# Kernel optimization log

Hardware: AMD Instinct MI355X
Metric: run time of the kernel (lower is better)

Reference implementation:

```python
import jax, jax.numpy as jnp
import numpy as np

EMBED_DIM = 768
NUM_HEADS = 8
HEAD_DIM = EMBED_DIM // NUM_HEADS
WINDOW_HALF = (17 - 1) // 2          # window_size=17 -> 8
GAP = 3 + 1                          # dilation_gap=3 -> stride 4
OVERLAP = WINDOW_HALF * GAP          # 32
N_LINES = 8192


def setup_inputs() -> dict:
    key = jax.random.key(0)
    k1, k2, k3, k4, k5 = jax.random.split(key, 5)
    D = EMBED_DIM
    return {
        "main": jax.random.normal(k1, (N_LINES, D), dtype=jnp.float32),
        "begin": jax.random.normal(k2, (OVERLAP, D), dtype=jnp.float32),
        "end": jax.random.normal(k3, (OVERLAP, D), dtype=jnp.float32),
        "in_proj_w": jax.random.normal(k4, (3 * D, D), dtype=jnp.float32) * 0.02,
        "in_proj_b": jnp.zeros((3 * D,), dtype=jnp.float32),
        "out_proj_w": jax.random.normal(k5, (D, D), dtype=jnp.float32) * 0.02,
        "out_proj_b": jnp.zeros((D,), dtype=jnp.float32),
    }


def reference(main, begin, end, in_proj_w, in_proj_b, out_proj_w, out_proj_b):
    N, D = main.shape
    H, hd = NUM_HEADS, HEAD_DIM
    # combined buffer [begin | main | end]; the per-token shifted concatenations
    # in the torch loop are equivalent to a strided gather into this buffer.
    combined = jnp.concatenate([begin, main, end], axis=0)  # [N + 2*OVERLAP, D]
    offsets = jnp.concatenate([
        jnp.arange(-OVERLAP, 0, GAP),
        jnp.arange(GAP, OVERLAP + GAP, GAP),
    ])  # [2*WINDOW_HALF] = [16]
    idx = jnp.arange(N)[:, None] + OVERLAP + offsets[None, :]  # [N, W]
    keys = combined[idx]  # [N, W, D] dilated window keys (= values)

    wq, wk, wv = in_proj_w[:D], in_proj_w[D:2 * D], in_proj_w[2 * D:]
    bq, bk, bv = in_proj_b[:D], in_proj_b[D:2 * D], in_proj_b[2 * D:]

    q = (main @ wq.T + bq).reshape(N, H, hd) * (hd ** -0.5)   # [N,H,hd]
    k = (keys @ wk.T + bk).reshape(N, -1, H, hd)              # [N,W,H,hd]
    v = (keys @ wv.T + bv).reshape(N, -1, H, hd)              # [N,W,H,hd]

    scores = jnp.einsum('nhd,nwhd->nhw', q, k)                # [N,H,W]
    attn = jax.nn.softmax(scores, axis=-1)
    ctx = jnp.einsum('nhw,nwhd->nhd', attn, v).reshape(N, D)
    attn_out = ctx @ out_proj_w.T + out_proj_b                # [N,D]
    return jnp.concatenate([main, attn_out], axis=-1)         # [N,2D]
```

## Files before the change

kernel.cpp:

```cpp
#include <hip/hip_runtime.h>
#include <math.h>

#define D 768
#define NQKV 2304
#define NH 8
#define HD 96
#define NW 16
#define OVL 32
#define NLINES 8192
#define NCOMB 8256
#define MPAD 8320
#define CH 64
#define SCALE_Q 0.1020620726159657f
#define COMB_BLOCKS 6240

typedef int i32x8 __attribute__((ext_vector_type(8)));
typedef float f32x4 __attribute__((ext_vector_type(4)));
typedef float f32x2 __attribute__((ext_vector_type(2)));

__device__ __forceinline__ unsigned int pk_fp8x4(float a, float b, float c, float d) {
    int u = __builtin_amdgcn_cvt_pk_fp8_f32(a, b, 0, false);
    u = __builtin_amdgcn_cvt_pk_fp8_f32(c, d, u, true);
    return (unsigned int)u;
}
__device__ __forceinline__ unsigned char f2fp8(float v) {
    return (unsigned char)(__builtin_amdgcn_cvt_pk_fp8_f32(v, v, 0, false) & 0xFF);
}
template <bool HI>
__device__ __forceinline__ f32x2 upk(unsigned int u) {
    return __builtin_amdgcn_cvt_pk_f32_fp8((int)u, HI);
}
__device__ __forceinline__ float dot4f8(unsigned int a, unsigned int b) {
    const f32x2 al = upk<false>(a), ah = upk<true>(a);
    const f32x2 bl = upk<false>(b), bh = upk<true>(b);
    return al.x * bl.x + al.y * bl.y + ah.x * bh.x + ah.y * bh.y;
}

__device__ __forceinline__ void stage16(const void* g, void* l) {
    __builtin_amdgcn_global_load_lds(
        (const __attribute__((address_space(1))) unsigned int*)g,
        (__attribute__((address_space(3))) unsigned int*)l, 16, 0, 0);
}

__device__ __forceinline__ void stage_sw(const unsigned char* gbase, unsigned char* lds, int ch) {
    const int row = ch >> 3;
    const int half = ch & 1;
    const int o = (((ch >> 1) & 3) - row) & 3;
    stage16(gbase + (size_t)row * D + o * 32 + half * 16, lds + ch * 16);
}

__device__ __forceinline__ int xcd_swz(int lin, int nwg) {
    const int q = nwg >> 3, r = nwg & 7;
    const int x = lin & 7, i = lin >> 3;
    return (x < r ? x * (q + 1) : r * (q + 1) + (x - r) * q) + i;
}

__global__ __launch_bounds__(256) void convert_all(const float* __restrict__ main_,
                                                   const float* __restrict__ begin_,
                                                   const float* __restrict__ end_,
                                                   const float* __restrict__ in_w,
                                                   const float* __restrict__ in_b,
                                                   const float* __restrict__ out_w,
                                                   unsigned int* __restrict__ comb_dst,
                                                   unsigned int* __restrict__ w_dst,
                                                   float* __restrict__ bias_s,
                                                   float* __restrict__ out) {
    const int bid = blockIdx.x;
    if (bid < COMB_BLOCKS) {
        const int i = bid * 256 + threadIdx.x;
        const int row = i / 192, c4 = i % 192;
        float4 v = make_float4(0.f, 0.f, 0.f, 0.f);
        if (row < NCOMB) {
            const float* src = (row < OVL) ? begin_ + (size_t)row * D
                             : (row < OVL + NLINES) ? main_ + (size_t)(row - OVL) * D
                                                    : end_ + (size_t)(row - OVL - NLINES) * D;
            v = *(const float4*)(src + c4 * 4);
            if (row >= OVL && row < OVL + NLINES)
                *(float4*)(out + (size_t)(row - OVL) * (2 * D) + c4 * 4) = v;
        }
        comb_dst[(size_t)row * 192 + c4] = pk_fp8x4(v.x, v.y, v.z, v.w);
    } else {
        const int j = (bid - COMB_BLOCKS) * 256 + threadIdx.x;
        const int f0 = j * 4;
        const bool is_out = f0 >= 3 * D * D;
        const float4 v = is_out ? *(const float4*)(out_w + (f0 - 3 * D * D))
                                : *(const float4*)(in_w + f0);
        const float s = 16.0f * ((f0 < D * D) ? SCALE_Q : 1.0f);
        w_dst[j] = pk_fp8x4(v.x * s, v.y * s, v.z * s, v.w * s);
        if (bid == COMB_BLOCKS) {
            for (int b = threadIdx.x; b < NQKV; b += 256)
                bias_s[b] = in_b[b] * (b < D ? SCALE_Q : 1.0f);
        }
    }
}

__global__ __launch_bounds__(256) void qkv_gemm(const unsigned char* __restrict__ comb,
                                                const unsigned char* __restrict__ w_f8,
                                                const float* __restrict__ bias_s,
                                                unsigned char* __restrict__ Qb,
                                                unsigned char* __restrict__ Kb,
                                                unsigned char* __restrict__ Vb) {
    __shared__ __align__(16) unsigned char As[2][128 * 128];
    __shared__ __align__(16) unsigned char Bs[2][128 * 128];
    const int lin = blockIdx.y * 18 + blockIdx.x;
    const int s = xcd_swz(lin, 18 * 65);
    const int bx = s % 18;
    const int m0 = (s / 18) * 128;
    const int n0 = bx * 128;
    const int tid = threadIdx.x;
    const int lane = tid & 63;
    const int wave = tid >> 6;
    const int wm = (wave & 1) * 64, wn = (wave >> 1) * 64;
    const int q = lane >> 4, l15 = lane & 15;
    const int swq = (q + l15) & 3;

#pragma unroll
    for (int it = 0; it < 4; it++) {
        const int ch = tid + it * 256;
        stage_sw(comb + (size_t)m0 * D, As[0], ch);
        stage_sw(w_f8 + (size_t)n0 * D, Bs[0], ch);
    }

    f32x4 acc[4][4] = {};
    int cur = 0;
    for (int k0 = 0; k0 < D; k0 += 128) {
        if (k0 + 128 < D) {
#pragma unroll
            for (int it = 0; it < 4; it++) {
                const int ch = tid + it * 256;
                stage_sw(comb + (size_t)m0 * D + k0 + 128, As[cur ^ 1], ch);
                stage_sw(w_f8 + (size_t)n0 * D + k0 + 128, Bs[cur ^ 1], ch);
            }
            asm volatile("s_waitcnt vmcnt(8)" ::: "memory");
        } else {
            asm volatile("s_waitcnt vmcnt(0)" ::: "memory");
        }
        __builtin_amdgcn_sched_barrier(0);
        __builtin_amdgcn_s_barrier();
        __builtin_amdgcn_sched_barrier(0);

        i32x8 af[4], bfr[4];
#pragma unroll
        for (int i = 0; i < 4; i++)
            af[i] = *(const i32x8*)(As[cur] + (wm + i * 16 + l15) * 128 + swq * 32);
#pragma unroll
        for (int j = 0; j < 4; j++)
            bfr[j] = *(const i32x8*)(Bs[cur] + (wn + j * 16 + l15) * 128 + swq * 32);
#pragma unroll
        for (int i = 0; i < 4; i++)
#pragma unroll
            for (int j = 0; j < 4; j++)
                acc[i][j] = __builtin_amdgcn_mfma_scale_f32_16x16x128_f8f6f4(
                    af[i], bfr[j], acc[i][j], 0, 0, 0, 127, 0, 123);

        asm volatile("s_waitcnt lgkmcnt(0)" ::: "memory");
        __builtin_amdgcn_sched_barrier(0);
        __builtin_amdgcn_s_barrier();
        __builtin_amdgcn_sched_barrier(0);
        cur ^= 1;
    }

    unsigned char* Cb = (bx < 6) ? Qb : (bx < 12 ? Kb : Vb);
    const int nloc = (bx % 6) * 128;
#pragma unroll
    for (int i = 0; i < 4; i++)
#pragma unroll
        for (int j = 0; j < 4; j++)
#pragma unroll
            for (int r = 0; r < 4; r++) {
                const int row = m0 + wm + i * 16 + q * 4 + r;
                const int col = wn + j * 16 + l15;
                Cb[(size_t)row * D + nloc + col] = f2fp8(acc[i][j][r] + bias_s[bx * 128 + col]);
            }
}

__global__ __launch_bounds__(256) void out_gemm(const unsigned char* __restrict__ ctx,
                                                const unsigned char* __restrict__ w,
                                                const float* __restrict__ bias,
                                                float* __restrict__ out) {
    __shared__ __align__(16) unsigned char As[2][64 * 128];
    __shared__ __align__(16) unsigned char Bs[2][128 * 128];
    const int lin = blockIdx.y * 6 + blockIdx.x;
    const int s = xcd_swz(lin, 6 * 128);
    const int m0 = (s / 6) * 64;
    const int n0 = (s % 6) * 128;
    const int tid = threadIdx.x;
    const int lane = tid & 63;
    const int wave = tid >> 6;
    const int wn = wave * 32;
    const int q = lane >> 4, l15 = lane & 15;
    const int swq = (q + l15) & 3;

#pragma unroll
    for (int it = 0; it < 2; it++)
        stage_sw(ctx + (size_t)m0 * D, As[0], tid + it * 256);
#pragma unroll
    for (int it = 0; it < 4; it++)
        stage_sw(w + (size_t)n0 * D, Bs[0], tid + it * 256);

    f32x4 acc[4][2] = {};
    int cur = 0;
    for (int k0 = 0; k0 < D; k0 += 128) {
        if (k0 + 128 < D) {
#pragma unroll
            for (int it = 0; it < 2; it++)
                stage_sw(ctx + (size_t)m0 * D + k0 + 128, As[cur ^ 1], tid + it * 256);
#pragma unroll
            for (int it = 0; it < 4; it++)
                stage_sw(w + (size_t)n0 * D + k0 + 128, Bs[cur ^ 1], tid + it * 256);
            asm volatile("s_waitcnt vmcnt(6)" ::: "memory");
        } else {
            asm volatile("s_waitcnt vmcnt(0)" ::: "memory");
        }
        __builtin_amdgcn_sched_barrier(0);
        __builtin_amdgcn_s_barrier();
        __builtin_amdgcn_sched_barrier(0);

        i32x8 af[4], bfr[2];
#pragma unroll
        for (int i = 0; i < 4; i++)
            af[i] = *(const i32x8*)(As[cur] + (i * 16 + l15) * 128 + swq * 32);
#pragma unroll
        for (int j = 0; j < 2; j++)
            bfr[j] = *(const i32x8*)(Bs[cur] + (wn + j * 16 + l15) * 128 + swq * 32);
#pragma unroll
        for (int i = 0; i < 4; i++)
#pragma unroll
            for (int j = 0; j < 2; j++)
                acc[i][j] = __builtin_amdgcn_mfma_scale_f32_16x16x128_f8f6f4(
                    af[i], bfr[j], acc[i][j], 0, 0, 0, 127, 0, 123);

        asm volatile("s_waitcnt lgkmcnt(0)" ::: "memory");
        __builtin_amdgcn_sched_barrier(0);
        __builtin_amdgcn_s_barrier();
        __builtin_amdgcn_sched_barrier(0);
        cur ^= 1;
    }

#pragma unroll
    for (int i = 0; i < 4; i++)
#pragma unroll
        for (int j = 0; j < 2; j++)
#pragma unroll
            for (int r = 0; r < 4; r++) {
                const int row = m0 + i * 16 + q * 4 + r;
                const int col = n0 + wn + j * 16 + l15;
                out[(size_t)row * (2 * D) + D + col] = acc[i][j][r] + bias[col];
            }
}

__global__ __launch_bounds__(256) void attn_kernel(const unsigned char* __restrict__ Q,
                                                   const unsigned char* __restrict__ K,
                                                   const unsigned char* __restrict__ V,
                                                   unsigned char* __restrict__ ctx) {
    const int lin = blockIdx.y * 128 + blockIdx.x;
    const int s = xcd_swz(lin, 128 * 8);
    const int n0 = (s % 128) * CH;
    const int h = s / 128;
    const int tid = threadIdx.x;

    __shared__ __align__(16) unsigned char sK[128 * 128];
    __shared__ __align__(16) unsigned char sV[128 * 128];
    __shared__ float sS[CH][17];

    const int l = tid & 63;
    const int wg = tid >> 6;

#pragma unroll
    for (int it = 0; it < 3; it++) {
        const int idx = tid + it * 256;
        const int row = idx / 6, c = idx % 6;
        const int slot = (c + row) & 7;
        *(uint4*)(sK + row * 128 + slot * 16) =
            *(const uint4*)(K + (size_t)(n0 + row) * D + h * HD + c * 16);
        *(uint4*)(sV + row * 128 + slot * 16) =
            *(const uint4*)(V + (size_t)(n0 + row) * D + h * HD + c * 16);
    }
    uint4 qreg[6];
#pragma unroll
    for (int c = 0; c < 6; c++)
        qreg[c] = *(const uint4*)(Q + (size_t)(n0 + l) * D + h * HD + c * 16);
    __syncthreads();

#pragma unroll
    for (int wi = 0; wi < 4; wi++) {
        const int w = wg * 4 + wi;
        const int lrow = l + 4 * w + (w >= 8 ? 4 : 0);
        float sc = 0.f;
#pragma unroll
        for (int c = 0; c < 6; c++) {
            const uint4 ka = *(const uint4*)(sK + lrow * 128 + ((c + lrow) & 7) * 16);
            sc += dot4f8(qreg[c].x, ka.x) + dot4f8(qreg[c].y, ka.y) +
                  dot4f8(qreg[c].z, ka.z) + dot4f8(qreg[c].w, ka.w);
        }
        sS[l][w] = sc;
    }
    __syncthreads();

    if (tid < CH) {
        float mx = -1e30f;
#pragma unroll
        for (int i = 0; i < NW; i++) mx = fmaxf(mx, sS[tid][i]);
        float e[NW], sum = 0.f;
#pragma unroll
        for (int i = 0; i < NW; i++) {
            e[i] = __expf(sS[tid][i] - mx);
            sum += e[i];
        }
        const float inv = 1.f / sum;
#pragma unroll
        for (int i = 0; i < NW; i++) sS[tid][i] = e[i] * inv;
    }
    __syncthreads();

    float p[NW];
#pragma unroll
    for (int i = 0; i < NW; i++) p[i] = sS[l][i];
    float acc[24] = {};
#pragma unroll
    for (int i = 0; i < NW; i++) {
        const int lrow = l + 4 * i + (i >= 8 ? 4 : 0);
        const unsigned char* vrow = sV + lrow * 128;
        const float pw = p[i];
#pragma unroll
        for (int c = 0; c < 3; c++) {
            const int off = wg * 24 + c * 8;
            const uint2 vv =
                *(const uint2*)(vrow + (((off >> 4) + lrow) & 7) * 16 + (off & 15));
            const f32x2 a0 = upk<false>(vv.x), a1 = upk<true>(vv.x);
            const f32x2 a2 = upk<false>(vv.y), a3 = upk<true>(vv.y);
            acc[c * 8 + 0] += pw * a0.x;
            acc[c * 8 + 1] += pw * a0.y;
            acc[c * 8 + 2] += pw * a1.x;
            acc[c * 8 + 3] += pw * a1.y;
            acc[c * 8 + 4] += pw * a2.x;
            acc[c * 8 + 5] += pw * a2.y;
            acc[c * 8 + 6] += pw * a3.x;
            acc[c * 8 + 7] += pw * a3.y;
        }
    }
    unsigned char* op = ctx + (size_t)(n0 + l) * D + h * HD + wg * 24;
#pragma unroll
    for (int c = 0; c < 3; c++) {
        const unsigned int u0 =
            pk_fp8x4(acc[c * 8 + 0], acc[c * 8 + 1], acc[c * 8 + 2], acc[c * 8 + 3]);
        const unsigned int u1 =
            pk_fp8x4(acc[c * 8 + 4], acc[c * 8 + 5], acc[c * 8 + 6], acc[c * 8 + 7]);
        *(uint2*)(op + c * 8) = make_uint2(u0, u1);
    }
}

extern "C" void kernel_launch(void* const* d_in, const int* in_sizes, int n_in,
                              void* d_out, int out_size, void* d_ws, size_t ws_size,
                              hipStream_t stream) {
    const float* main_ = (const float*)d_in[0];
    const float* begin_ = (const float*)d_in[1];
    const float* end_ = (const float*)d_in[2];
    const float* in_w = (const float*)d_in[3];
    const float* in_b = (const float*)d_in[4];
    const float* out_w = (const float*)d_in[5];
    const float* out_b = (const float*)d_in[6];
    float* out = (float*)d_out;

    unsigned char* comb_f8 = (unsigned char*)d_ws;
    unsigned char* w_f8 = comb_f8 + (size_t)MPAD * D;
    unsigned char* Qb = w_f8 + (size_t)4 * D * D;
    unsigned char* Kb = Qb + (size_t)MPAD * D;
    unsigned char* Vb = Kb + (size_t)MPAD * D;
    unsigned char* ctx_f8 = Vb + (size_t)MPAD * D;
    float* bias_s = (float*)(ctx_f8 + (size_t)NLINES * D);

    convert_all<<<COMB_BLOCKS + 4 * D * D / 1024, 256, 0, stream>>>(
        main_, begin_, end_, in_w, in_b, out_w, (unsigned int*)comb_f8,
        (unsigned int*)w_f8, bias_s, out);
    qkv_gemm<<<dim3(18, 65), 256, 0, stream>>>(comb_f8, w_f8, bias_s, Qb, Kb, Vb);
    attn_kernel<<<dim3(128, NH), 256, 0, stream>>>(Qb + (size_t)OVL * D, Kb, Vb, ctx_f8);
    out_gemm<<<dim3(6, 128), 256, 0, stream>>>(ctx_f8, w_f8 + (size_t)3 * D * D,
                                               out_b, out);
}
```

Before: 160.6 us.

## Compute attention scores with FP8 MFMA over a banded tile and wave-level softmax

The QK score computation now stages Q and K tiles into LDS with direct global-to-LDS loads, zero-padding head dim 96 to 128 from a zero row. Each wave computes a 16x128 band of the 64x128 score matrix with scaled FP8 16x16x128 MFMA and keeps only the dilated-window diagonals. Softmax runs in registers with cross-lane shuffles instead of a single 64-thread serial pass. This replaces scalar fp8 unpack-dot loops, at the cost of computing many masked-out scores and relying on the padding region being zero.

Result: faster. 147.1 us (-8.4%).

```diff
diff --git a/kernel.cpp b/kernel.cpp
--- a/kernel.cpp
+++ b/kernel.cpp
@@ -13,6 +13,7 @@
 #define CH 64
 #define SCALE_Q 0.1020620726159657f
 #define COMB_BLOCKS 6240
+#define CONV_BLOCKS (COMB_BLOCKS + 4 * D * D / 1024)
 
 typedef int i32x8 __attribute__((ext_vector_type(8)));
 typedef float f32x4 __attribute__((ext_vector_type(4)));
@@ -29,11 +30,6 @@
 template <bool HI>
 __device__ __forceinline__ f32x2 upk(unsigned int u) {
     return __builtin_amdgcn_cvt_pk_f32_fp8((int)u, HI);
-}
-__device__ __forceinline__ float dot4f8(unsigned int a, unsigned int b) {
-    const f32x2 al = upk<false>(a), ah = upk<true>(a);
-    const f32x2 bl = upk<false>(b), bh = upk<true>(b);
-    return al.x * bl.x + al.y * bl.y + ah.x * bh.x + ah.y * bh.y;
 }
 
 __device__ __forceinline__ void stage16(const void* g, void* l) {
@@ -49,10 +45,26 @@
     stage16(gbase + (size_t)row * D + o * 32 + half * 16, lds + ch * 16);
 }
 
+__device__ __forceinline__ void stage96(const unsigned char* growbase, size_t rstride,
+                                        const unsigned char* zrow, unsigned char* lds, int ch) {
+    const int row = ch >> 3;
+    const int half = ch & 1;
+    const int o = (((ch >> 1) & 3) - row) & 3;
+    const unsigned char* src = (o < 3) ? growbase + (size_t)row * rstride + o * 32 + half * 16
+                                       : zrow + half * 16;
+    stage16(src, lds + ch * 16);
+}
+
 __device__ __forceinline__ int xcd_swz(int lin, int nwg) {
     const int q = nwg >> 3, r = nwg & 7;
     const int x = lin & 7, i = lin >> 3;
     return (x < r ? x * (q + 1) : r * (q + 1) + (x - r) * q) + i;
+}
+
+__device__ __forceinline__ float sel4(f32x4 v, int r) {
+    const float ab = (r & 1) ? v.y : v.x;
+    const float cd = (r & 1) ? v.w : v.z;
+    return (r & 2) ? cd : ab;
 }
 
 __global__ __launch_bounds__(256) void convert_all(const float* __restrict__ main_,
@@ -249,73 +261,87 @@
             }
 }
 
-__global__ __launch_bounds__(256) void attn_kernel(const unsigned char* __restrict__ Q,
-                                                   const unsigned char* __restrict__ K,
-                                                   const unsigned char* __restrict__ V,
-                                                   unsigned char* __restrict__ ctx) {
+__global__ __launch_bounds__(256, 4) void attn_kernel(const unsigned char* __restrict__ Q,
+                                                      const unsigned char* __restrict__ K,
+                                                      const unsigned char* __restrict__ V,
+                                                      const unsigned char* __restrict__ zrow,
+                                                      unsigned char* __restrict__ ctx) {
     const int lin = blockIdx.y * 128 + blockIdx.x;
     const int s = xcd_swz(lin, 128 * 8);
     const int n0 = (s % 128) * CH;
     const int h = s / 128;
     const int tid = threadIdx.x;
 
-    __shared__ __align__(16) unsigned char sK[128 * 128];
-    __shared__ __align__(16) unsigned char sV[128 * 128];
-    __shared__ float sS[CH][17];
+    __shared__ __align__(16) unsigned char pool[40960];
+    unsigned char* sK = pool;
+    unsigned char* sV = pool + 16384;
+    unsigned char* sQ = pool + 32768;
+    float* sS = (float*)(pool + 32768);
 
     const int l = tid & 63;
     const int wg = tid >> 6;
+    const int q = l >> 4, l15 = l & 15;
 
 #pragma unroll
     for (int it = 0; it < 3; it++) {
         const int idx = tid + it * 256;
         const int row = idx / 6, c = idx % 6;
         const int slot = (c + row) & 7;
-        *(uint4*)(sK + row * 128 + slot * 16) =
-            *(const uint4*)(K + (size_t)(n0 + row) * D + h * HD + c * 16);
         *(uint4*)(sV + row * 128 + slot * 16) =
             *(const uint4*)(V + (size_t)(n0 + row) * D + h * HD + c * 16);
     }
-    uint4 qreg[6];
-#pragma unroll
-    for (int c = 0; c < 6; c++)
-        qreg[c] = *(const uint4*)(Q + (size_t)(n0 + l) * D + h * HD + c * 16);
+#pragma unroll
+    for (int it = 0; it < 4; it++)
+        stage96(K + (size_t)n0 * D + h * HD, D, zrow, sK, tid + it * 256);
+#pragma unroll
+    for (int it = 0; it < 2; it++)
+        stage96(Q + (size_t)n0 * D + h * HD, D, zrow, sQ, tid + it * 256);
     __syncthreads();
 
-#pragma unroll
-    for (int wi = 0; wi < 4; wi++) {
-        const int w = wg * 4 + wi;
-        const int lrow = l + 4 * w + (w >= 8 ? 4 : 0);
-        float sc = 0.f;
-#pragma unroll
-        for (int c = 0; c < 6; c++) {
-            const uint4 ka = *(const uint4*)(sK + lrow * 128 + ((c + lrow) & 7) * 16);
-            sc += dot4f8(qreg[c].x, ka.x) + dot4f8(qreg[c].y, ka.y) +
-                  dot4f8(qreg[c].z, ka.z) + dot4f8(qreg[c].w, ka.w);
-        }
-        sS[l][w] = sc;
-    }
+    const i32x8 af = *(const i32x8*)(sQ + (wg * 16 + l15) * 128 + ((q + l15) & 3) * 32);
     __syncthreads();
 
-    if (tid < CH) {
-        float mx = -1e30f;
-#pragma unroll
-        for (int i = 0; i < NW; i++) mx = fmaxf(mx, sS[tid][i]);
-        float e[NW], sum = 0.f;
-#pragma unroll
-        for (int i = 0; i < NW; i++) {
-            e[i] = __expf(sS[tid][i] - mx);
-            sum += e[i];
-        }
-        const float inv = 1.f / sum;
-#pragma unroll
-        for (int i = 0; i < NW; i++) sS[tid][i] = e[i] * inv;
+    const int rstar = l15 & 3;
+    const int e = (l15 >> 2) - q;
+    const int mq = wg * 16 + q * 4 + rstar;
+    float sc[8];
+    float mx = -1e30f;
+#pragma unroll
+    for (int j = 0; j < 8; j++) {
+        const i32x8 bf = *(const i32x8*)(sK + (j * 16 + l15) * 128 + ((q + l15) & 3) * 32);
+        f32x4 z = {};
+        const f32x4 a = __builtin_amdgcn_mfma_scale_f32_16x16x128_f8f6f4(
+            af, bf, z, 0, 0, 0, 127, 0, 127);
+        const int d4 = 4 * (j - wg) + e;
+        const bool valid = (d4 >= 0) & (d4 <= 16) & (d4 != 8);
+        sc[j] = valid ? sel4(a, rstar) : -1e30f;
+        mx = fmaxf(mx, sc[j]);
+    }
+    mx = fmaxf(mx, __shfl_xor(mx, 4));
+    mx = fmaxf(mx, __shfl_xor(mx, 8));
+    float sum = 0.f;
+    float pr[8];
+#pragma unroll
+    for (int j = 0; j < 8; j++) {
+        pr[j] = __expf(sc[j] - mx);
+        sum += pr[j];
+    }
+    sum += __shfl_xor(sum, 4);
+    sum += __shfl_xor(sum, 8);
+    const float inv = 1.f / sum;
+#pragma unroll
+    for (int j = 0; j < 8; j++) {
+        const int d4 = 4 * (j - wg) + e;
+        if ((d4 >= 0) & (d4 <= 16) & (d4 != 8)) {
+            const int win = (d4 < 8) ? d4 : d4 - 1;
+            sS[mq * 17 + win] = pr[j] * inv;
+        }
     }
     __syncthreads();
 
     float p[NW];
 #pragma unroll
-    for (int i = 0; i < NW; i++) p[i] = sS[l][i];
+    for (int i = 0; i < NW; i++) p[i] = sS[l * 17 + i];
     float acc[24] = {};
 #pragma unroll
     for (int i = 0; i < NW; i++) {
@@ -369,12 +395,14 @@
     unsigned char* Vb = Kb + (size_t)MPAD * D;
     unsigned char* ctx_f8 = Vb + (size_t)MPAD * D;
     float* bias_s = (float*)(ctx_f8 + (size_t)NLINES * D);
-
-    convert_all<<<COMB_BLOCKS + 4 * D * D / 1024, 256, 0, stream>>>(
+    unsigned char* zrow = comb_f8 + (size_t)NCOMB * D;
+
+    convert_all<<<CONV_BLOCKS, 256, 0, stream>>>(
         main_, begin_, end_, in_w, in_b, out_w, (unsigned int*)comb_f8,
         (unsigned int*)w_f8, bias_s, out);
     qkv_gemm<<<dim3(18, 65), 256, 0, stream>>>(comb_f8, w_f8, bias_s, Qb, Kb, Vb);
-    attn_kernel<<<dim3(128, NH), 256, 0, stream>>>(Qb + (size_t)OVL * D, Kb, Vb, ctx_f8);
+    attn_kernel<<<dim3(128, NH), 256, 0, stream>>>(Qb + (size_t)OVL * D, Kb, Vb, zrow,
+                                                   ctx_f8);
     out_gemm<<<dim3(6, 128), 256, 0, stream>>>(ctx_f8, w_f8 + (size_t)3 * D * D,
                                                out_b, out);
 }
```
